# Optimization experiments

Measured on AMD Instinct MI355X. Metric: run time of the kernel, lower is better.

Reference implementation:

```python
import jax, jax.numpy as jnp
import numpy as np

NH, DK, DV = 8, 10, 10  # num_heads, per-head key dim, per-head value dim (dim_k=dim_v=80)


def setup_inputs() -> dict:
    key = jax.random.key(0)
    k1, k2, k3, k4, k5 = jax.random.split(key, 5)
    B, NX, NY = 64, 512, 512
    x = jax.random.normal(k1, (B, NX, 768), dtype=jnp.float32)
    y = jax.random.normal(k2, (B, NY, 283), dtype=jnp.float32)
    # nn.Linear(bias=False) weights, stored transposed as (in, out); scaled init
    Wq = jax.random.normal(k3, (768, 80), dtype=jnp.float32) * 0.02
    Wk = jax.random.normal(k4, (283, 80), dtype=jnp.float32) * 0.02
    Wv = jax.random.normal(k5, (283, 80), dtype=jnp.float32) * 0.02
    return {"x": x, "y": y, "Wq": Wq, "Wk": Wk, "Wv": Wv}


def reference(x, y, Wq, Wk, Wv):
    B, nx, _ = x.shape
    ny = y.shape[1]
    # projections -> split heads: (B, nh, seq, dhead)
    q = (x @ Wq).reshape(B, nx, NH, DK).transpose(0, 2, 1, 3)
    k = (y @ Wk).reshape(B, ny, NH, DK).transpose(0, 2, 1, 3)
    v = (y @ Wv).reshape(B, ny, NH, DV).transpose(0, 2, 1, 3)
    scale = 1.0 / np.sqrt(DK).astype(np.float32)
    dist = jax.nn.softmax(jnp.einsum("bhqd,bhkd->bhqk", q, k) * scale, axis=-1)
    att = q + jnp.einsum("bhqk,bhkd->bhqd", dist, v)  # residual add of q
    att = att.transpose(0, 2, 1, 3).reshape(B, nx, NH * DV)
    # module returns `result` = flattened attention (fc/BN stack is dead code)
    return att.reshape(B, -1)
```

## Files before the change

### kernel.cpp

```cpp
#include <hip/hip_runtime.h>
#include <stdint.h>

typedef unsigned short u16;
typedef unsigned int   u32;
typedef _Float16       f16;

typedef __attribute__((ext_vector_type(2))) _Float16 half2v;
typedef __attribute__((ext_vector_type(4))) _Float16 half4v;
typedef __attribute__((ext_vector_type(8))) _Float16 half8v;
typedef __attribute__((ext_vector_type(4))) float    floatx4;

#define NXS    512
#define NYS    512
#define NHEAD  8
#define DHEAD  10
#define DMODEL 80
#define DXK    768
#define DYK    283
#define DYKP   288

__device__ inline half2v pk2(float x, float y) {
  return __builtin_bit_cast(half2v, __builtin_amdgcn_cvt_pkrtz(x, y));
}
__device__ inline half4v cvt4(float4 v) {
  return __builtin_shufflevector(pk2(v.x, v.y), pk2(v.z, v.w), 0, 1, 2, 3);
}
__device__ inline half4v h4u32(u32 a, u32 b) {
  return __builtin_shufflevector(__builtin_bit_cast(half2v, a),
                                 __builtin_bit_cast(half2v, b), 0, 1, 2, 3);
}

__global__ __launch_bounds__(256) void w_prep(const float* __restrict__ Wq,
                                              const float* __restrict__ Wk,
                                              const float* __restrict__ Wv,
                                              f16* __restrict__ Tq,
                                              f16* __restrict__ Tk,
                                              f16* __restrict__ Tv) {
  const int idx = blockIdx.x * 256 + threadIdx.x;
  if (idx < 80 * 768) {
    const int c = idx / 768, k = idx - c * 768;
    Tq[idx] = (f16)Wq[k * 80 + c];
  }
  if (idx < 80 * 288) {
    const int c = idx / 288, k = idx - c * 288;
    float a = 0.f, b = 0.f;
    if (k < DYK) { a = Wk[k * 80 + c]; b = Wv[k * 80 + c]; }
    Tk[idx] = (f16)a;
    Tv[idx] = (f16)b;
  }
}

__global__ __launch_bounds__(256) void proj(const float* __restrict__ X,
                                            const float* __restrict__ Y,
                                            const f16* __restrict__ Wtq,
                                            const f16* __restrict__ Wtk,
                                            const f16* __restrict__ Wtv,
                                            f16* __restrict__ Qw,
                                            f16* __restrict__ Kw,
                                            f16* __restrict__ Vw) {
  const int t = threadIdx.x;
  const int wv = t >> 6, lane = t & 63, m16 = lane & 15, quad = lane >> 4;
  const int blk = blockIdx.x;

  if (blk < 512) {
    __shared__ f16 Xs[64 * 40];
    __shared__ f16 Ws[80 * 40];
    const int row0 = blk * 64;
    const int xr_r = t >> 3, xr_k = (t & 7) << 2;
    const int wi0 = t, wi1 = t + 160;

    float4 xr0, xr1;
    uint4 wr0, wr1;
    xr0 = *(const float4*)&X[(size_t)(row0 + xr_r) * DXK + xr_k];
    xr1 = *(const float4*)&X[(size_t)(row0 + xr_r + 32) * DXK + xr_k];
    if (t < 160) {
      wr0 = *(const uint4*)&Wtq[(wi0 >> 2) * DXK + (wi0 & 3) * 8];
      wr1 = *(const uint4*)&Wtq[(wi1 >> 2) * DXK + (wi1 & 3) * 8];
    }

    floatx4 acc[5];
#pragma unroll
    for (int i = 0; i < 5; ++i) acc[i] = (floatx4){0.f, 0.f, 0.f, 0.f};

    for (int s = 0; s < 24; ++s) {
      if (s) __syncthreads();
      *(half4v*)&Xs[xr_r * 40 + xr_k] = cvt4(xr0);
      *(half4v*)&Xs[(xr_r + 32) * 40 + xr_k] = cvt4(xr1);
      if (t < 160) {
        *(uint4*)&Ws[(wi0 >> 2) * 40 + (wi0 & 3) * 8] = wr0;
        *(uint4*)&Ws[(wi1 >> 2) * 40 + (wi1 & 3) * 8] = wr1;
      }
      __syncthreads();
      if (s < 23) {
        const int k0 = (s + 1) * 32;
        xr0 = *(const float4*)&X[(size_t)(row0 + xr_r) * DXK + k0 + xr_k];
        xr1 = *(const float4*)&X[(size_t)(row0 + xr_r + 32) * DXK + k0 + xr_k];
        if (t < 160) {
          wr0 = *(const uint4*)&Wtq[(wi0 >> 2) * DXK + k0 + (wi0 & 3) * 8];
          wr1 = *(const uint4*)&Wtq[(wi1 >> 2) * DXK + k0 + (wi1 & 3) * 8];
        }
      }
      const half8v a = *(const half8v*)&Xs[(wv * 16 + m16) * 40 + quad * 8];
#pragma unroll
      for (int nt = 0; nt < 5; ++nt) {
        const half8v b = *(const half8v*)&Ws[(nt * 16 + m16) * 40 + quad * 8];
        acc[nt] = __builtin_amdgcn_mfma_f32_16x16x32_f16(a, b, acc[nt], 0, 0, 0);
      }
    }
#pragma unroll
    for (int nt = 0; nt < 5; ++nt) {
      const int col = nt * 16 + m16;
#pragma unroll
      for (int p = 0; p < 4; ++p) {
        const int grow = row0 + wv * 16 + quad * 4 + p;
        Qw[(size_t)grow * DMODEL + col] = (f16)acc[nt][p];
      }
    }
  } else {
    __shared__ f16 Ys[64 * 40];
    __shared__ f16 Wks[80 * 40];
    __shared__ f16 Wvs[80 * 40];
    const int row0 = (blk - 512) * 64;
    const int wi0 = t, wi1 = t + 160;

    float yr[8];
    uint4 wk0, wk1, wv0, wv1;
#pragma unroll
    for (int i = 0; i < 8; ++i) {
      const int idx = t + 256 * i;
      const int r = idx >> 5, kk = idx & 31;
      yr[i] = Y[(size_t)(row0 + r) * DYK + kk];
    }
    if (t < 160) {
      wk0 = *(const uint4*)&Wtk[(wi0 >> 2) * DYKP + (wi0 & 3) * 8];
      wk1 = *(const uint4*)&Wtk[(wi1 >> 2) * DYKP + (wi1 & 3) * 8];
      wv0 = *(const uint4*)&Wtv[(wi0 >> 2) * DYKP + (wi0 & 3) * 8];
      wv1 = *(const uint4*)&Wtv[(wi1 >> 2) * DYKP + (wi1 & 3) * 8];
    }

    floatx4 ak[5], av[5];
#pragma unroll
    for (int i = 0; i < 5; ++i) {
      ak[i] = (floatx4){0.f, 0.f, 0.f, 0.f};
      av[i] = (floatx4){0.f, 0.f, 0.f, 0.f};
    }

    for (int s = 0; s < 9; ++s) {
      if (s) __syncthreads();
#pragma unroll
      for (int i = 0; i < 8; ++i) {
        const int idx = t + 256 * i;
        Ys[(idx >> 5) * 40 + (idx & 31)] = (f16)yr[i];
      }
      if (t < 160) {
        *(uint4*)&Wks[(wi0 >> 2) * 40 + (wi0 & 3) * 8] = wk0;
        *(uint4*)&Wks[(wi1 >> 2) * 40 + (wi1 & 3) * 8] = wk1;
        *(uint4*)&Wvs[(wi0 >> 2) * 40 + (wi0 & 3) * 8] = wv0;
        *(uint4*)&Wvs[(wi1 >> 2) * 40 + (wi1 & 3) * 8] = wv1;
      }
      __syncthreads();
      if (s < 8) {
        const int k0 = (s + 1) * 32;
#pragma unroll
        for (int i = 0; i < 8; ++i) {
          const int idx = t + 256 * i;
          const int r = idx >> 5, k = k0 + (idx & 31);
          yr[i] = (k < DYK) ? Y[(size_t)(row0 + r) * DYK + k] : 0.f;
        }
        if (t < 160) {
          wk0 = *(const uint4*)&Wtk[(wi0 >> 2) * DYKP + k0 + (wi0 & 3) * 8];
          wk1 = *(const uint4*)&Wtk[(wi1 >> 2) * DYKP + k0 + (wi1 & 3) * 8];
          wv0 = *(const uint4*)&Wtv[(wi0 >> 2) * DYKP + k0 + (wi0 & 3) * 8];
          wv1 = *(const uint4*)&Wtv[(wi1 >> 2) * DYKP + k0 + (wi1 & 3) * 8];
        }
      }
      const half8v a = *(const half8v*)&Ys[(wv * 16 + m16) * 40 + quad * 8];
#pragma unroll
      for (int nt = 0; nt < 5; ++nt) {
        const half8v bk = *(const half8v*)&Wks[(nt * 16 + m16) * 40 + quad * 8];
        ak[nt] = __builtin_amdgcn_mfma_f32_16x16x32_f16(a, bk, ak[nt], 0, 0, 0);
        const half8v bv = *(const half8v*)&Wvs[(nt * 16 + m16) * 40 + quad * 8];
        av[nt] = __builtin_amdgcn_mfma_f32_16x16x32_f16(a, bv, av[nt], 0, 0, 0);
      }
    }
#pragma unroll
    for (int nt = 0; nt < 5; ++nt) {
      const int col = nt * 16 + m16;
      const int h = col / 10, d = col - h * 10;
#pragma unroll
      for (int p = 0; p < 4; ++p) {
        const int grow = row0 + wv * 16 + quad * 4 + p;
        const int bb = grow >> 9, ny = grow & 511;
        const size_t o = (((size_t)bb * NHEAD + h) * NYS + ny) * DHEAD + d;
        Kw[o] = (f16)ak[nt][p];
        Vw[o] = (f16)av[nt][p];
      }
    }
  }
}

__global__ __launch_bounds__(256) void attn(const f16* __restrict__ Q,
                                            const f16* __restrict__ K,
                                            const f16* __restrict__ V,
                                            float* __restrict__ O) {
  __shared__ f16 Ks[512 * 22];
  __shared__ f16 Vt[16 * 522];
  const int t = threadIdx.x;
  const int wv = t >> 6, lane = t & 63, m16 = lane & 15, quad = lane >> 4;
  const int bh = blockIdx.x >> 1, half = blockIdx.x & 1;
  const int b = bh >> 3, h = bh & 7;

  const u32* Kg = (const u32*)K + (size_t)bh * NYS * 5;
  const u32* Vg = (const u32*)V + (size_t)bh * NYS * 5;
  for (int idx = t; idx < 2560; idx += 256) {
    const u32 row = (u32)idx / 5u, c = (u32)idx - row * 5u;
    const half2v kv = __builtin_bit_cast(half2v, Kg[idx]);
    Ks[row * 22 + 2 * c]     = kv[0];
    Ks[row * 22 + 2 * c + 1] = kv[1];
    const half2v vvv = __builtin_bit_cast(half2v, Vg[idx]);
    Vt[(2 * c) * 522 + row]     = vvv[0];
    Vt[(2 * c + 1) * 522 + row] = vvv[1];
  }
  for (int idx = t; idx < 3072; idx += 256) {
    const u32 row = (u32)idx / 6u, d = 10u + ((u32)idx - row * 6u);
    Ks[row * 22 + d] = (f16)0.f;
  }
  for (int idx = t; idx < 6 * 522; idx += 256)
    Vt[10 * 522 + idx] = (f16)0.f;
  __syncthreads();

  const float scale = 0.31622776601683794f;
#pragma unroll 1
  for (int i = 0; i < 4; ++i) {
    const int qt = half * 16 + wv * 4 + i;
    const int qrow = qt * 16 + m16;
    const u32* Qg32 = (const u32*)(Q + ((size_t)b * NXS + qrow) * DMODEL + h * DHEAD);
    float s0 = 0.f, s1 = 0.f, s2 = 0.f, s3 = 0.f;
    if (quad < 2) {
      const u32 ua = Qg32[quad * 2], ub = Qg32[quad * 2 + 1];
      const half2v ha = __builtin_bit_cast(half2v, ua);
      const half2v hb = __builtin_bit_cast(half2v, ub);
      s0 = (float)ha[0]; s1 = (float)ha[1]; s2 = (float)hb[0]; s3 = (float)hb[1];
    } else if (quad == 2) {
      const u32 ua = Qg32[4];
      const half2v ha = __builtin_bit_cast(half2v, ua);
      s0 = (float)ha[0]; s1 = (float)ha[1];
    }
    const half4v qf = __builtin_shufflevector(pk2(s0 * scale, s1 * scale),
                                              pk2(s2 * scale, s3 * scale),
                                              0, 1, 2, 3);
    floatx4 o0 = (floatx4){0.f, 0.f, 0.f, 0.f};
    floatx4 o1 = (floatx4){0.f, 0.f, 0.f, 0.f};
    float l0 = 0.f, l1 = 0.f;
    for (int kt = 0; kt < 32; kt += 2) {
#pragma unroll
      for (int u = 0; u < 2; ++u) {
        const int ktu = kt + u;
        const int kb = (ktu * 16 + m16) * 22 + quad * 4;
        const half4v kf = h4u32(*(const u32*)&Ks[kb], *(const u32*)&Ks[kb + 2]);
        const floatx4 s = __builtin_amdgcn_mfma_f32_16x16x16f16(
            kf, qf, (floatx4){0.f, 0.f, 0.f, 0.f}, 0, 0, 0);
        const float p0 = __expf(s[0]);
        const float p1 = __expf(s[1]);
        const float p2 = __expf(s[2]);
        const float p3 = __expf(s[3]);
        const half4v pf = __builtin_shufflevector(pk2(p0, p1), pk2(p2, p3),
                                                  0, 1, 2, 3);
        const int vb = m16 * 522 + ktu * 16 + quad * 4;
        const half4v vf = h4u32(*(const u32*)&Vt[vb], *(const u32*)&Vt[vb + 2]);
        if (u == 0) {
          l0 += (p0 + p1) + (p2 + p3);
          o0 = __builtin_amdgcn_mfma_f32_16x16x16f16(pf, vf, o0, 0, 0, 0);
        } else {
          l1 += (p0 + p1) + (p2 + p3);
          o1 = __builtin_amdgcn_mfma_f32_16x16x16f16(pf, vf, o1, 0, 0, 0);
        }
      }
    }
    float lp = l0 + l1;
    lp += __shfl_xor(lp, 16);
    lp += __shfl_xor(lp, 32);
#pragma unroll
    for (int p = 0; p < 4; ++p) {
      const int rq = qt * 16 + quad * 4 + p;
      const float lr = __shfl(lp, quad * 4 + p);
      if (m16 < DHEAD) {
        const float qres = (float)Q[((size_t)b * NXS + rq) * DMODEL + h * DHEAD + m16];
        O[((size_t)b * NXS + rq) * DMODEL + h * DHEAD + m16] =
            qres + (o0[p] + o1[p]) / lr;
      }
    }
  }
}

extern "C" void kernel_launch(void* const* d_in, const int* in_sizes, int n_in,
                              void* d_out, int out_size, void* d_ws, size_t ws_size,
                              hipStream_t stream) {
  const float* x  = (const float*)d_in[0];
  const float* y  = (const float*)d_in[1];
  const float* Wq = (const float*)d_in[2];
  const float* Wk = (const float*)d_in[3];
  const float* Wv = (const float*)d_in[4];
  float* out = (float*)d_out;

  char* ws = (char*)d_ws;
  f16* Wtq = (f16*)(ws);
  f16* Wtk = (f16*)(ws + 122880);
  f16* Wtv = (f16*)(ws + 168960);
  f16* Qw  = (f16*)(ws + 262144);
  f16* Kw  = (f16*)(ws + 5505024);
  f16* Vw  = (f16*)(ws + 10747904);

  w_prep<<<240, 256, 0, stream>>>(Wq, Wk, Wv, Wtq, Wtk, Wtv);
  proj  <<<1024, 256, 0, stream>>>(x, y, Wtq, Wtk, Wtv, Qw, Kw, Vw);
  attn  <<<1024, 256, 0, stream>>>(Qw, Kw, Vw, out);
}
```

Before: 239.0 us.

## Fuse weight prep, projection and attention into one cooperative persistent kernel

Merges the three kernels (weight transpose, QKV projection, attention) into a single cooperative kernel that uses grid-wide syncs between phases. Blocks loop persistently over the former work items, with grid size set from occupancy times CU count. The aim is to remove two kernel launch gaps and tail effects. In exchange it adds grid-sync cost, and the shared union smem sized for attention (~39 KB) may lower occupancy during the projection phase.

```diff
diff --git a/kernel.cpp b/kernel.cpp
--- a/kernel.cpp
+++ b/kernel.cpp
@@ -1,5 +1,8 @@
 #include <hip/hip_runtime.h>
+#include <hip/hip_cooperative_groups.h>
 #include <stdint.h>
+
+namespace cg = cooperative_groups;
 
 typedef unsigned short u16;
 typedef unsigned int   u32;
@@ -30,264 +33,262 @@
                                  __builtin_bit_cast(half2v, b), 0, 1, 2, 3);
 }
 
-__global__ __launch_bounds__(256) void w_prep(const float* __restrict__ Wq,
-                                              const float* __restrict__ Wk,
-                                              const float* __restrict__ Wv,
-                                              f16* __restrict__ Tq,
-                                              f16* __restrict__ Tk,
-                                              f16* __restrict__ Tv) {
-  const int idx = blockIdx.x * 256 + threadIdx.x;
-  if (idx < 80 * 768) {
+__global__ __launch_bounds__(256) void fused(const float* __restrict__ X,
+                                             const float* __restrict__ Y,
+                                             const float* __restrict__ Wq,
+                                             const float* __restrict__ Wk,
+                                             const float* __restrict__ Wv,
+                                             f16* __restrict__ Wtq,
+                                             f16* __restrict__ Wtk,
+                                             f16* __restrict__ Wtv,
+                                             f16* __restrict__ Qw,
+                                             f16* __restrict__ Kw,
+                                             f16* __restrict__ Vw,
+                                             float* __restrict__ O) {
+  __shared__ f16 smem[19616];
+  cg::grid_group grid = cg::this_grid();
+  const int t = threadIdx.x;
+  const int wv = t >> 6, lane = t & 63, m16 = lane & 15, quad = lane >> 4;
+
+  for (int idx = blockIdx.x * 256 + t; idx < 80 * 768; idx += gridDim.x * 256) {
     const int c = idx / 768, k = idx - c * 768;
-    Tq[idx] = (f16)Wq[k * 80 + c];
-  }
-  if (idx < 80 * 288) {
+    Wtq[idx] = (f16)Wq[k * 80 + c];
+  }
+  for (int idx = blockIdx.x * 256 + t; idx < 80 * 288; idx += gridDim.x * 256) {
     const int c = idx / 288, k = idx - c * 288;
     float a = 0.f, b = 0.f;
     if (k < DYK) { a = Wk[k * 80 + c]; b = Wv[k * 80 + c]; }
-    Tk[idx] = (f16)a;
-    Tv[idx] = (f16)b;
-  }
-}
-
-__global__ __launch_bounds__(256) void proj(const float* __restrict__ X,
-                                            const float* __restrict__ Y,
-                                            const f16* __restrict__ Wtq,
-                                            const f16* __restrict__ Wtk,
-                                            const f16* __restrict__ Wtv,
-                                            f16* __restrict__ Qw,
-                                            f16* __restrict__ Kw,
-                                            f16* __restrict__ Vw) {
-  const int t = threadIdx.x;
-  const int wv = t >> 6, lane = t & 63, m16 = lane & 15, quad = lane >> 4;
-  const int blk = blockIdx.x;
-
-  if (blk < 512) {
-    __shared__ f16 Xs[64 * 40];
-    __shared__ f16 Ws[80 * 40];
-    const int row0 = blk * 64;
-    const int xr_r = t >> 3, xr_k = (t & 7) << 2;
-    const int wi0 = t, wi1 = t + 160;
-
-    float4 xr0, xr1;
-    uint4 wr0, wr1;
-    xr0 = *(const float4*)&X[(size_t)(row0 + xr_r) * DXK + xr_k];
-    xr1 = *(const float4*)&X[(size_t)(row0 + xr_r + 32) * DXK + xr_k];
-    if (t < 160) {
-      wr0 = *(const uint4*)&Wtq[(wi0 >> 2) * DXK + (wi0 & 3) * 8];
-      wr1 = *(const uint4*)&Wtq[(wi1 >> 2) * DXK + (wi1 & 3) * 8];
-    }
-
-    floatx4 acc[5];
-#pragma unroll
-    for (int i = 0; i < 5; ++i) acc[i] = (floatx4){0.f, 0.f, 0.f, 0.f};
-
-    for (int s = 0; s < 24; ++s) {
-      if (s) __syncthreads();
-      *(half4v*)&Xs[xr_r * 40 + xr_k] = cvt4(xr0);
-      *(half4v*)&Xs[(xr_r + 32) * 40 + xr_k] = cvt4(xr1);
+    Wtk[idx] = (f16)a;
+    Wtv[idx] = (f16)b;
+  }
+  grid.sync();
+
+  for (int pb = blockIdx.x; pb < 1024; pb += gridDim.x) {
+    __syncthreads();
+    if (pb < 512) {
+      f16* const Xs = smem;
+      f16* const Ws = smem + 2560;
+      const int row0 = pb * 64;
+      const int xr_r = t >> 3, xr_k = (t & 7) << 2;
+      const int wi0 = t, wi1 = t + 160;
+
+      float4 xr0, xr1;
+      uint4 wr0, wr1;
+      xr0 = *(const float4*)&X[(size_t)(row0 + xr_r) * DXK + xr_k];
+      xr1 = *(const float4*)&X[(size_t)(row0 + xr_r + 32) * DXK + xr_k];
       if (t < 160) {
-        *(uint4*)&Ws[(wi0 >> 2) * 40 + (wi0 & 3) * 8] = wr0;
-        *(uint4*)&Ws[(wi1 >> 2) * 40 + (wi1 & 3) * 8] = wr1;
-      }
-      __syncthreads();
-      if (s < 23) {
-        const int k0 = (s + 1) * 32;
-        xr0 = *(const float4*)&X[(size_t)(row0 + xr_r) * DXK + k0 + xr_k];
-        xr1 = *(const float4*)&X[(size_t)(row0 + xr_r + 32) * DXK + k0 + xr_k];
+        wr0 = *(const uint4*)&Wtq[(wi0 >> 2) * DXK + (wi0 & 3) * 8];
+        wr1 = *(const uint4*)&Wtq[(wi1 >> 2) * DXK + (wi1 & 3) * 8];
+      }
+
+      floatx4 acc[5];
+#pragma unroll
+      for (int i = 0; i < 5; ++i) acc[i] = (floatx4){0.f, 0.f, 0.f, 0.f};
+
+      for (int s = 0; s < 24; ++s) {
+        if (s) __syncthreads();
+        *(half4v*)&Xs[xr_r * 40 + xr_k] = cvt4(xr0);
+        *(half4v*)&Xs[(xr_r + 32) * 40 + xr_k] = cvt4(xr1);
         if (t < 160) {
-          wr0 = *(const uint4*)&Wtq[(wi0 >> 2) * DXK + k0 + (wi0 & 3) * 8];
-          wr1 = *(const uint4*)&Wtq[(wi1 >> 2) * DXK + k0 + (wi1 & 3) * 8];
-        }
-      }
-      const half8v a = *(const half8v*)&Xs[(wv * 16 + m16) * 40 + quad * 8];
+          *(uint4*)&Ws[(wi0 >> 2) * 40 + (wi0 & 3) * 8] = wr0;
+          *(uint4*)&Ws[(wi1 >> 2) * 40 + (wi1 & 3) * 8] = wr1;
+        }
+        __syncthreads();
+        if (s < 23) {
+          const int k0 = (s + 1) * 32;
+          xr0 = *(const float4*)&X[(size_t)(row0 + xr_r) * DXK + k0 + xr_k];
+          xr1 = *(const float4*)&X[(size_t)(row0 + xr_r + 32) * DXK + k0 + xr_k];
+          if (t < 160) {
+            wr0 = *(const uint4*)&Wtq[(wi0 >> 2) * DXK + k0 + (wi0 & 3) * 8];
+            wr1 = *(const uint4*)&Wtq[(wi1 >> 2) * DXK + k0 + (wi1 & 3) * 8];
+          }
+        }
+        const half8v a = *(const half8v*)&Xs[(wv * 16 + m16) * 40 + quad * 8];
+#pragma unroll
+        for (int nt = 0; nt < 5; ++nt) {
+          const half8v b = *(const half8v*)&Ws[(nt * 16 + m16) * 40 + quad * 8];
+          acc[nt] = __builtin_amdgcn_mfma_f32_16x16x32_f16(a, b, acc[nt], 0, 0, 0);
+        }
+      }
 #pragma unroll
       for (int nt = 0; nt < 5; ++nt) {
-        const half8v b = *(const half8v*)&Ws[(nt * 16 + m16) * 40 + quad * 8];
-        acc[nt] = __builtin_amdgcn_mfma_f32_16x16x32_f16(a, b, acc[nt], 0, 0, 0);
-      }
-    }
-#pragma unroll
-    for (int nt = 0; nt < 5; ++nt) {
-      const int col = nt * 16 + m16;
-#pragma unroll
-      for (int p = 0; p < 4; ++p) {
-        const int grow = row0 + wv * 16 + quad * 4 + p;
-        Qw[(size_t)grow * DMODEL + col] = (f16)acc[nt][p];
-      }
-    }
-  } else {
-    __shared__ f16 Ys[64 * 40];
-    __shared__ f16 Wks[80 * 40];
-    __shared__ f16 Wvs[80 * 40];
-    const int row0 = (blk - 512) * 64;
-    const int wi0 = t, wi1 = t + 160;
-
-    float yr[8];
-    uint4 wk0, wk1, wv0, wv1;
-#pragma unroll
-    for (int i = 0; i < 8; ++i) {
-      const int idx = t + 256 * i;
-      const int r = idx >> 5, kk = idx & 31;
-      yr[i] = Y[(size_t)(row0 + r) * DYK + kk];
-    }
-    if (t < 160) {
-      wk0 = *(const uint4*)&Wtk[(wi0 >> 2) * DYKP + (wi0 & 3) * 8];
-      wk1 = *(const uint4*)&Wtk[(wi1 >> 2) * DYKP + (wi1 & 3) * 8];
-      wv0 = *(const uint4*)&Wtv[(wi0 >> 2) * DYKP + (wi0 & 3) * 8];
-      wv1 = *(const uint4*)&Wtv[(wi1 >> 2) * DYKP + (wi1 & 3) * 8];
-    }
-
-    floatx4 ak[5], av[5];
-#pragma unroll
-    for (int i = 0; i < 5; ++i) {
-      ak[i] = (floatx4){0.f, 0.f, 0.f, 0.f};
-      av[i] = (floatx4){0.f, 0.f, 0.f, 0.f};
-    }
-
-    for (int s = 0; s < 9; ++s) {
-      if (s) __syncthreads();
+        const int col = nt * 16 + m16;
+#pragma unroll
+        for (int p = 0; p < 4; ++p) {
+          const int grow = row0 + wv * 16 + quad * 4 + p;
+          Qw[(size_t)grow * DMODEL + col] = (f16)acc[nt][p];
+        }
+      }
+    } else {
+      f16* const Ys  = smem;
+      f16* const Wks = smem + 2560;
+      f16* const Wvs = smem + 5760;
+      const int row0 = (pb - 512) * 64;
+      const int wi0 = t, wi1 = t + 160;
+
+      float yr[8];
+      uint4 wk0, wk1, wv0, wv1;
 #pragma unroll
       for (int i = 0; i < 8; ++i) {
         const int idx = t + 256 * i;
-        Ys[(idx >> 5) * 40 + (idx & 31)] = (f16)yr[i];
+        const int r = idx >> 5, kk = idx & 31;
+        yr[i] = Y[(size_t)(row0 + r) * DYK + kk];
       }
       if (t < 160) {
-        *(uint4*)&Wks[(wi0 >> 2) * 40 + (wi0 & 3) * 8] = wk0;
-        *(uint4*)&Wks[(wi1 >> 2) * 40 + (wi1 & 3) * 8] = wk1;
-        *(uint4*)&Wvs[(wi0 >> 2) * 40 + (wi0 & 3) * 8] = wv0;
-        *(uint4*)&Wvs[(wi1 >> 2) * 40 + (wi1 & 3) * 8] = wv1;
-      }
-      __syncthreads();
-      if (s < 8) {
-        const int k0 = (s + 1) * 32;
+        wk0 = *(const uint4*)&Wtk[(wi0 >> 2) * DYKP + (wi0 & 3) * 8];
+        wk1 = *(const uint4*)&Wtk[(wi1 >> 2) * DYKP + (wi1 & 3) * 8];
+        wv0 = *(const uint4*)&Wtv[(wi0 >> 2) * DYKP + (wi0 & 3) * 8];
+        wv1 = *(const uint4*)&Wtv[(wi1 >> 2) * DYKP + (wi1 & 3) * 8];
+      }
+
+      floatx4 ak[5], av[5];
+#pragma unroll
+      for (int i = 0; i < 5; ++i) {
+        ak[i] = (floatx4){0.f, 0.f, 0.f, 0.f};
+        av[i] = (floatx4){0.f, 0.f, 0.f, 0.f};
+      }
+
+      for (int s = 0; s < 9; ++s) {
+        if (s) __syncthreads();
 #pragma unroll
         for (int i = 0; i < 8; ++i) {
           const int idx = t + 256 * i;
-          const int r = idx >> 5, k = k0 + (idx & 31);
-          yr[i] = (k < DYK) ? Y[(size_t)(row0 + r) * DYK + k] : 0.f;
+          Ys[(idx >> 5) * 40 + (idx & 31)] = (f16)yr[i];
         }
         if (t < 160) {
-          wk0 = *(const uint4*)&Wtk[(wi0 >> 2) * DYKP + k0 + (wi0 & 3) * 8];
-          wk1 = *(const uint4*)&Wtk[(wi1 >> 2) * DYKP + k0 + (wi1 & 3) * 8];
-          wv0 = *(const uint4*)&Wtv[(wi0 >> 2) * DYKP + k0 + (wi0 & 3) * 8];
-          wv1 = *(const uint4*)&Wtv[(wi1 >> 2) * DYKP + k0 + (wi1 & 3) * 8];
-        }
-      }
-      const half8v a = *(const half8v*)&Ys[(wv * 16 + m16) * 40 + quad * 8];
+          *(uint4*)&Wks[(wi0 >> 2) * 40 + (wi0 & 3) * 8] = wk0;
+          *(uint4*)&Wks[(wi1 >> 2) * 40 + (wi1 & 3) * 8] = wk1;
+          *(uint4*)&Wvs[(wi0 >> 2) * 40 + (wi0 & 3) * 8] = wv0;
+          *(uint4*)&Wvs[(wi1 >> 2) * 40 + (wi1 & 3) * 8] = wv1;
+        }
+        __syncthreads();
+        if (s < 8) {
+          const int k0 = (s + 1) * 32;
+#pragma unroll
+          for (int i = 0; i < 8; ++i) {
+            const int idx = t + 256 * i;
+            const int r = idx >> 5, k = k0 + (idx & 31);
+            yr[i] = (k < DYK) ? Y[(size_t)(row0 + r) * DYK + k] : 0.f;
+          }
+          if (t < 160) {
+            wk0 = *(const uint4*)&Wtk[(wi0 >> 2) * DYKP + k0 + (wi0 & 3) * 8];
+            wk1 = *(const uint4*)&Wtk[(wi1 >> 2) * DYKP + k0 + (wi1 & 3) * 8];
+            wv0 = *(const uint4*)&Wtv[(wi0 >> 2) * DYKP + k0 + (wi0 & 3) * 8];
+            wv1 = *(const uint4*)&Wtv[(wi1 >> 2) * DYKP + k0 + (wi1 & 3) * 8];
+          }
+        }
+        const half8v a = *(const half8v*)&Ys[(wv * 16 + m16) * 40 + quad * 8];
+#pragma unroll
+        for (int nt = 0; nt < 5; ++nt) {
+          const half8v bk = *(const half8v*)&Wks[(nt * 16 + m16) * 40 + quad * 8];
+          ak[nt] = __builtin_amdgcn_mfma_f32_16x16x32_f16(a, bk, ak[nt], 0, 0, 0);
+          const half8v bv = *(const half8v*)&Wvs[(nt * 16 + m16) * 40 + quad * 8];
+          av[nt] = __builtin_amdgcn_mfma_f32_16x16x32_f16(a, bv, av[nt], 0, 0, 0);
+        }
+      }
 #pragma unroll
       for (int nt = 0; nt < 5; ++nt) {
-        const half8v bk = *(const half8v*)&Wks[(nt * 16 + m16) * 40 + quad * 8];
-        ak[nt] = __builtin_amdgcn_mfma_f32_16x16x32_f16(a, bk, ak[nt], 0, 0, 0);
-        const half8v bv = *(const half8v*)&Wvs[(nt * 16 + m16) * 40 + quad * 8];
-        av[nt] = __builtin_amdgcn_mfma_f32_16x16x32_f16(a, bv, av[nt], 0, 0, 0);
+        const int col = nt * 16 + m16;
+        const int h = col / 10, d = col - h * 10;
+#pragma unroll
+        for (int p = 0; p < 4; ++p) {
+          const int grow = row0 + wv * 16 + quad * 4 + p;
+          const int bb = grow >> 9, ny = grow & 511;
+          const size_t o = (((size_t)bb * NHEAD + h) * NYS + ny) * DHEAD + d;
+          Kw[o] = (f16)ak[nt][p];
+          Vw[o] = (f16)av[nt][p];
+        }
       }
     }
-#pragma unroll
-    for (int nt = 0; nt < 5; ++nt) {
-      const int col = nt * 16 + m16;
-      const int h = col / 10, d = col - h * 10;
+  }
+  grid.sync();
+
+  for (int ab = blockIdx.x; ab < 1024; ab += gridDim.x) {
+    __syncthreads();
+    f16* const Ks = smem;
+    f16* const Vt = smem + 11264;
+    const int bh = ab >> 1, hf = ab & 1;
+    const int b = bh >> 3, h = bh & 7;
+
+    const u32* Kg = (const u32*)Kw + (size_t)bh * NYS * 5;
+    const u32* Vg = (const u32*)Vw + (size_t)bh * NYS * 5;
+    for (int idx = t; idx < 2560; idx += 256) {
+      const u32 row = (u32)idx / 5u, c = (u32)idx - row * 5u;
+      const half2v kv = __builtin_bit_cast(half2v, Kg[idx]);
+      Ks[row * 22 + 2 * c]     = kv[0];
+      Ks[row * 22 + 2 * c + 1] = kv[1];
+      const half2v vvv = __builtin_bit_cast(half2v, Vg[idx]);
+      Vt[(2 * c) * 522 + row]     = vvv[0];
+      Vt[(2 * c + 1) * 522 + row] = vvv[1];
+    }
+    for (int idx = t; idx < 3072; idx += 256) {
+      const u32 row = (u32)idx / 6u, d = 10u + ((u32)idx - row * 6u);
+      Ks[row * 22 + d] = (f16)0.f;
+    }
+    for (int idx = t; idx < 6 * 522; idx += 256)
+      Vt[10 * 522 + idx] = (f16)0.f;
+    __syncthreads();
+
+    const float scale = 0.31622776601683794f;
+#pragma unroll 1
+    for (int i = 0; i < 4; ++i) {
+      const int qt = hf * 16 + wv * 4 + i;
+      const int qrow = qt * 16 + m16;
+      const u32* Qg32 = (const u32*)(Qw + ((size_t)b * NXS + qrow) * DMODEL + h * DHEAD);
+      float s0 = 0.f, s1 = 0.f, s2 = 0.f, s3 = 0.f;
+      if (quad < 2) {
+        const u32 ua = Qg32[quad * 2], ub = Qg32[quad * 2 + 1];
+        const half2v ha = __builtin_bit_cast(half2v, ua);
+        const half2v hb = __builtin_bit_cast(half2v, ub);
+        s0 = (float)ha[0]; s1 = (float)ha[1]; s2 = (float)hb[0]; s3 = (float)hb[1];
+      } else if (quad == 2) {
+        const u32 ua = Qg32[4];
+        const half2v ha = __builtin_bit_cast(half2v, ua);
+        s0 = (float)ha[0]; s1 = (float)ha[1];
+      }
+      const half4v qf = __builtin_shufflevector(pk2(s0 * scale, s1 * scale),
+                                                pk2(s2 * scale, s3 * scale),
+                                                0, 1, 2, 3);
+      floatx4 o0 = (floatx4){0.f, 0.f, 0.f, 0.f};
+      floatx4 o1 = (floatx4){0.f, 0.f, 0.f, 0.f};
+      float l0 = 0.f, l1 = 0.f;
+      for (int kt = 0; kt < 32; kt += 2) {
+#pragma unroll
+        for (int u = 0; u < 2; ++u) {
+          const int ktu = kt + u;
+          const int kb = (ktu * 16 + m16) * 22 + quad * 4;
+          const half4v kf = h4u32(*(const u32*)&Ks[kb], *(const u32*)&Ks[kb + 2]);
+          const floatx4 s = __builtin_amdgcn_mfma_f32_16x16x16f16(
+              kf, qf, (floatx4){0.f, 0.f, 0.f, 0.f}, 0, 0, 0);
+          const float p0 = __expf(s[0]);
+          const float p1 = __expf(s[1]);
+          const float p2 = __expf(s[2]);
+          const float p3 = __expf(s[3]);
+          const half4v pf = __builtin_shufflevector(pk2(p0, p1), pk2(p2, p3),
+                                                    0, 1, 2, 3);
+          const int vb = m16 * 522 + ktu * 16 + quad * 4;
+          const half4v vf = h4u32(*(const u32*)&Vt[vb], *(const u32*)&Vt[vb + 2]);
+          if (u == 0) {
+            l0 += (p0 + p1) + (p2 + p3);
+            o0 = __builtin_amdgcn_mfma_f32_16x16x16f16(pf, vf, o0, 0, 0, 0);
+          } else {
+            l1 += (p0 + p1) + (p2 + p3);
+            o1 = __builtin_amdgcn_mfma_f32_16x16x16f16(pf, vf, o1, 0, 0, 0);
+          }
+        }
+      }
+      float lp = l0 + l1;
+      lp += __shfl_xor(lp, 16);
+      lp += __shfl_xor(lp, 32);
 #pragma unroll
       for (int p = 0; p < 4; ++p) {
-        const int grow = row0 + wv * 16 + quad * 4 + p;
-        const int bb = grow >> 9, ny = grow & 511;
-        const size_t o = (((size_t)bb * NHEAD + h) * NYS + ny) * DHEAD + d;
-        Kw[o] = (f16)ak[nt][p];
-        Vw[o] = (f16)av[nt][p];
-      }
-    }
-  }
-}
-
-__global__ __launch_bounds__(256) void attn(const f16* __restrict__ Q,
-                                            const f16* __restrict__ K,
-                                            const f16* __restrict__ V,
-                                            float* __restrict__ O) {
-  __shared__ f16 Ks[512 * 22];
-  __shared__ f16 Vt[16 * 522];
-  const int t = threadIdx.x;
-  const int wv = t >> 6, lane = t & 63, m16 = lane & 15, quad = lane >> 4;
-  const int bh = blockIdx.x >> 1, half = blockIdx.x & 1;
-  const int b = bh >> 3, h = bh & 7;
-
-  const u32* Kg = (const u32*)K + (size_t)bh * NYS * 5;
-  const u32* Vg = (const u32*)V + (size_t)bh * NYS * 5;
-  for (int idx = t; idx < 2560; idx += 256) {
-    const u32 row = (u32)idx / 5u, c = (u32)idx - row * 5u;
-    const half2v kv = __builtin_bit_cast(half2v, Kg[idx]);
-    Ks[row * 22 + 2 * c]     = kv[0];
-    Ks[row * 22 + 2 * c + 1] = kv[1];
-    const half2v vvv = __builtin_bit_cast(half2v, Vg[idx]);
-    Vt[(2 * c) * 522 + row]     = vvv[0];
-    Vt[(2 * c + 1) * 522 + row] = vvv[1];
-  }
-  for (int idx = t; idx < 3072; idx += 256) {
-    const u32 row = (u32)idx / 6u, d = 10u + ((u32)idx - row * 6u);
-    Ks[row * 22 + d] = (f16)0.f;
-  }
-  for (int idx = t; idx < 6 * 522; idx += 256)
-    Vt[10 * 522 + idx] = (f16)0.f;
-  __syncthreads();
-
-  const float scale = 0.31622776601683794f;
-#pragma unroll 1
-  for (int i = 0; i < 4; ++i) {
-    const int qt = half * 16 + wv * 4 + i;
-    const int qrow = qt * 16 + m16;
-    const u32* Qg32 = (const u32*)(Q + ((size_t)b * NXS + qrow) * DMODEL + h * DHEAD);
-    float s0 = 0.f, s1 = 0.f, s2 = 0.f, s3 = 0.f;
-    if (quad < 2) {
-      const u32 ua = Qg32[quad * 2], ub = Qg32[quad * 2 + 1];
-      const half2v ha = __builtin_bit_cast(half2v, ua);
-      const half2v hb = __builtin_bit_cast(half2v, ub);
-      s0 = (float)ha[0]; s1 = (float)ha[1]; s2 = (float)hb[0]; s3 = (float)hb[1];
-    } else if (quad == 2) {
-      const u32 ua = Qg32[4];
-      const half2v ha = __builtin_bit_cast(half2v, ua);
-      s0 = (float)ha[0]; s1 = (float)ha[1];
-    }
-    const half4v qf = __builtin_shufflevector(pk2(s0 * scale, s1 * scale),
-                                              pk2(s2 * scale, s3 * scale),
-                                              0, 1, 2, 3);
-    floatx4 o0 = (floatx4){0.f, 0.f, 0.f, 0.f};
-    floatx4 o1 = (floatx4){0.f, 0.f, 0.f, 0.f};
-    float l0 = 0.f, l1 = 0.f;
-    for (int kt = 0; kt < 32; kt += 2) {
-#pragma unroll
-      for (int u = 0; u < 2; ++u) {
-        const int ktu = kt + u;
-        const int kb = (ktu * 16 + m16) * 22 + quad * 4;
-        const half4v kf = h4u32(*(const u32*)&Ks[kb], *(const u32*)&Ks[kb + 2]);
-        const floatx4 s = __builtin_amdgcn_mfma_f32_16x16x16f16(
-            kf, qf, (floatx4){0.f, 0.f, 0.f, 0.f}, 0, 0, 0);
-        const float p0 = __expf(s[0]);
-        const float p1 = __expf(s[1]);
-        const float p2 = __expf(s[2]);
-        const float p3 = __expf(s[3]);
-        const half4v pf = __builtin_shufflevector(pk2(p0, p1), pk2(p2, p3),
-                                                  0, 1, 2, 3);
-        const int vb = m16 * 522 + ktu * 16 + quad * 4;
-        const half4v vf = h4u32(*(const u32*)&Vt[vb], *(const u32*)&Vt[vb + 2]);
-        if (u == 0) {
-          l0 += (p0 + p1) + (p2 + p3);
-          o0 = __builtin_amdgcn_mfma_f32_16x16x16f16(pf, vf, o0, 0, 0, 0);
-        } else {
-          l1 += (p0 + p1) + (p2 + p3);
-          o1 = __builtin_amdgcn_mfma_f32_16x16x16f16(pf, vf, o1, 0, 0, 0);
-        }
-      }
-    }
-    float lp = l0 + l1;
-    lp += __shfl_xor(lp, 16);
-    lp += __shfl_xor(lp, 32);
-#pragma unroll
-    for (int p = 0; p < 4; ++p) {
-      const int rq = qt * 16 + quad * 4 + p;
-      const float lr = __shfl(lp, quad * 4 + p);
-      if (m16 < DHEAD) {
-        const float qres = (float)Q[((size_t)b * NXS + rq) * DMODEL + h * DHEAD + m16];
-        O[((size_t)b * NXS + rq) * DMODEL + h * DHEAD + m16] =
-            qres + (o0[p] + o1[p]) / lr;
+        const int rq = qt * 16 + quad * 4 + p;
+        const float lr = __shfl(lp, quad * 4 + p);
+        if (m16 < DHEAD) {
+          const float qres = (float)Qw[((size_t)b * NXS + rq) * DMODEL + h * DHEAD + m16];
+          O[((size_t)b * NXS + rq) * DMODEL + h * DHEAD + m16] =
+              qres + (o0[p] + o1[p]) / lr;
+        }
       }
     }
   }
@@ -311,7 +312,25 @@
   f16* Kw  = (f16*)(ws + 5505024);
   f16* Vw  = (f16*)(ws + 10747904);
 
-  w_prep<<<240, 256, 0, stream>>>(Wq, Wk, Wv, Wtq, Wtk, Wtv);
-  proj  <<<1024, 256, 0, stream>>>(x, y, Wtq, Wtk, Wtv, Qw, Kw, Vw);
-  attn  <<<1024, 256, 0, stream>>>(Qw, Kw, Vw, out);
-}
+  static int gridBlocks = 0;
+  if (gridBlocks == 0) {
+    int perCU = 0;
+    if (hipOccupancyMaxActiveBlocksPerMultiprocessor(&perCU, fused, 256, 0)
+            != hipSuccess || perCU < 1)
+      perCU = 1;
+    hipDeviceProp_t prop;
+    int dev = 0;
+    hipGetDevice(&dev);
+    int numCU = (hipGetDeviceProperties(&prop, dev) == hipSuccess)
+                    ? prop.multiProcessorCount : 256;
+    long mb = (long)perCU * numCU;
+    gridBlocks = (mb < 1024) ? (int)mb : 1024;
+    if (gridBlocks < 1) gridBlocks = 1;
+  }
+
+  void* args[] = {(void*)&x, (void*)&y, (void*)&Wq, (void*)&Wk, (void*)&Wv,
+                  (void*)&Wtq, (void*)&Wtk, (void*)&Wtv,
+                  (void*)&Qw, (void*)&Kw, (void*)&Vw, (void*)&out};
+  hipLaunchCooperativeKernel((void*)fused, dim3(gridBlocks), dim3(256),
+                             args, 0, stream);
+}
```

Measured after the change: 362.3 us. 1.52x slower.
